# Optimization experiments

Measured on AMD Instinct MI355X. Metric: run time of the kernel, lower is better.

## Reference

```python
import jax, jax.numpy as jnp
import numpy as np

B, N, D, K = 4, 2048, 128, 32
EPS = 1e-5  # nn.LayerNorm default eps


def _lin(k, fan_in, fan_out):
    kw, kb = jax.random.split(k)
    s = 1.0 / np.sqrt(fan_in)
    w = jax.random.uniform(kw, (fan_in, fan_out), jnp.float32, -s, s)
    b = jax.random.uniform(kb, (fan_out,), jnp.float32, -s, s)
    return w, b


def setup_inputs() -> dict:
    key = jax.random.key(0)
    ks = jax.random.split(key, 3)
    inp = {}
    inp["features"] = jax.random.normal(ks[0], (B, N, D), jnp.float32)
    inp["coords"] = jax.random.uniform(ks[1], (B, N, 3), jnp.float32) * 64.0
    names = [("ql", D, D), ("kl", D, D), ("vl", D, D), ("pl1", 3, D), ("pl2", D, D),
             ("we1", D, D), ("we2", D, D), ("pe1", 3, D), ("pe2", D, D),
             ("sg1", D, D), ("sg2", D, D)]
    k2 = jax.random.split(ks[2], len(names))
    for (nm, fi, fo), kk in zip(names, k2):
        w, b = _lin(kk, fi, fo)
        inp[nm + "_w"] = w
        inp[nm + "_b"] = b
    inp["lnA_g"] = jnp.ones((D,), jnp.float32)
    inp["lnA_b"] = jnp.zeros((D,), jnp.float32)
    inp["lnF_g"] = jnp.ones((D,), jnp.float32)
    inp["lnF_b"] = jnp.zeros((D,), jnp.float32)
    return inp


def _sparsemax_k(z):
    # sparsemax over axis=1 (the K neighbor axis) of [N, K, D]
    zs = -jnp.sort(-z, axis=1)                      # descending sort
    zc = jnp.cumsum(zs, axis=1)
    r = jnp.arange(1, K + 1, dtype=z.dtype)[None, :, None]
    support = (r * zs) > (zc - 1.0)
    kz = jnp.sum(support, axis=1, keepdims=True).astype(jnp.int32)  # >= 1
    tau = (jnp.take_along_axis(zc, kz - 1, axis=1) - 1.0) / kz.astype(z.dtype)
    return jnp.maximum(z - tau, 0.0)


def _sg_prop(x, src, tgt, n):
    # SGConv (K=1) propagation: D^{-1/2}(A+I)D^{-1/2} x with self-loops added
    ar = jnp.arange(n)
    s = jnp.concatenate([src, ar])
    t = jnp.concatenate([tgt, ar])
    deg = jax.ops.segment_sum(jnp.ones(s.shape, x.dtype), t, num_segments=n)
    dinv = jax.lax.rsqrt(deg)
    norm = dinv[s] * dinv[t]
    return jax.ops.segment_sum(x[s] * norm[:, None], t, num_segments=n)


def reference(features, coords,
              ql_w, ql_b, kl_w, kl_b, vl_w, vl_b,
              pl1_w, pl1_b, pl2_w, pl2_b,
              we1_w, we1_b, we2_w, we2_b,
              lnA_g, lnA_b,
              pe1_w, pe1_b, pe2_w, pe2_b,
              sg1_w, sg1_b, sg2_w, sg2_b,
              lnF_g, lnF_b):
    def ln(x, g, b):
        m = jnp.mean(x, axis=-1, keepdims=True)
        v = jnp.var(x, axis=-1, keepdims=True)
        return (x - m) * jax.lax.rsqrt(v + EPS) * g + b

    def one(feat, coord):
        # ---- RNSA: KNN self-attention with positional embedding ----
        d2 = jnp.sum((coord[:, None, :] - coord[None, :, :]) ** 2, axis=-1)  # [N,N]
        _, idx = jax.lax.top_k(-d2, K)                   # [N,K], self included first
        diff = coord[idx] - coord[:, None, :]            # [N,K,3]
        fc = jnp.maximum(diff @ pl1_w + pl1_b, 0.0) @ pl2_w + pl2_b  # [N,K,D]
        pe = fc + feat[idx]
        Q = jnp.maximum(feat @ ql_w + ql_b, 0.0)         # [N,D]
        Kf = jnp.maximum(pe @ kl_w + kl_b, 0.0)          # [N,K,D]
        V = pe @ vl_w + vl_b
        rel = (Kf - Q[:, None, :]) * fc
        w = jnp.maximum(rel @ we1_w + we1_b, 0.0) @ we2_w + we2_b
        w = _sparsemax_k(w)                              # attn_drop is identity (eval)
        x_att = feat + jnp.einsum('nkd,nkd->nd', V, w)   # residual add
        cf = jnp.maximum(coord @ pe1_w + pe1_b, 0.0) @ pe2_w + pe2_b
        x_in = ln(x_att, lnA_g, lnA_b)
        x_pe = x_in + cf
        d2m = d2 + jnp.where(jnp.eye(N, dtype=bool), jnp.inf, 0.0)  # knn_graph: loop=False
        _, idx2 = jax.lax.top_k(-d2m, K)                 # [N,K] neighbors (sources)
        src = idx2.reshape(-1)
        tgt = jnp.repeat(jnp.arange(N), K)
        h = _sg_prop(x_pe, src, tgt, N) @ sg1_w + sg1_b
        h = jnp.maximum(h, 0.0)
        h = _sg_prop(h, src, tgt, N) @ sg2_w + sg2_b     # dropout is identity (eval)
        return ln(h + x_in, lnF_g, lnF_b)

    return jax.vmap(one)(features, coords)
```

## Files before the change

### kernel.cpp

```cpp
#include <hip/hip_runtime.h>
#include <hip/hip_bf16.h>


namespace {
constexpr int BB = 4;
constexpr int NN = 2048;
constexpr int DD = 128;
constexpr int KK = 32;
constexpr float LNEPS = 1e-5f;
constexpr int SH = 136;
constexpr int SF = 132;

constexpr int W_QL = 0, W_KL = 16384, W_VL = 32768, W_PL2 = 49152, W_WE1 = 65536,
              W_WE2 = 81920, W_PE2 = 98304, W_SG1 = 114688, W_SG2 = 131072,
              W_PL1 = 147456, W_PE1 = 147840,
              B_QL = 148224, B_KL = 148352, B_VL = 148480, B_PL1 = 148608, B_PL2 = 148736,
              B_WE1 = 148864, B_WE2 = 148992, B_PE1 = 149120, B_PE2 = 149248,
              B_SG1 = 149376, B_SG2 = 149504,
              LNA_G = 149632, LNA_B = 149760, LNF_G = 149888, LNF_B = 150016;

constexpr long OFF_FEAT  = 0;
constexpr long OFF_Q     = 1l << 20;
constexpr long OFF_XATT  = 2l << 20;
constexpr long OFF_XIN   = 3l << 20;
constexpr long OFF_XPE   = 4l << 20;
constexpr long OFF_H1    = 5l << 20;
constexpr long OFF_COORD = 6l << 20;
constexpr long OFF_W     = (6l << 20) + 32768;
constexpr long OFF_IDX   = (6l << 20) + 262144;
}

typedef __attribute__((ext_vector_type(8))) short short8;
typedef __attribute__((ext_vector_type(4))) float f32x4;

struct WPtrs { const void* p[26]; };

__device__ __forceinline__ unsigned short f2bf(float f) {
  unsigned u = __float_as_uint(f);
  return (unsigned short)((u + 0x7fffu + ((u >> 16) & 1u)) >> 16);
}
__device__ __forceinline__ float bf2f(unsigned short h) {
  return __uint_as_float(((unsigned)h) << 16);
}
__device__ __forceinline__ f32x4 mfma16(short8 a, short8 b, f32x4 c) {
  return __builtin_amdgcn_mfma_f32_16x16x32_bf16(a, b, c, 0, 0, 0);
}

__global__ void k_detect(const unsigned* __restrict__ lnAg, int* __restrict__ flag) {
  if (threadIdx.x == 0 && blockIdx.x == 0) *flag = ((lnAg[0] & 0xFFFFu) != 0u) ? 1 : 0;
}

__global__ __launch_bounds__(256) void k_convert_inputs(
    const void* __restrict__ feat, const void* __restrict__ coord, const int* __restrict__ flag,
    float* __restrict__ featf, float* __restrict__ coordf) {
  const bool isbf = (*flag != 0);
  const int nf = BB * NN * DD, nc = BB * NN * 3;
  for (int i = blockIdx.x * 256 + threadIdx.x; i < nf + nc; i += gridDim.x * 256) {
    if (i < nf) {
      featf[i] = isbf ? __bfloat162float(((const __hip_bfloat16*)feat)[i])
                      : ((const float*)feat)[i];
    } else {
      const int j = i - nf;
      coordf[j] = isbf ? __bfloat162float(((const __hip_bfloat16*)coord)[j])
                       : ((const float*)coord)[j];
    }
  }
}

__global__ __launch_bounds__(256) void k_convert_weights(WPtrs wp, const int* __restrict__ flag,
                                                         float* __restrict__ Wf) {
  const int sizes[26] = {16384,16384,16384,16384,16384,16384,16384,16384,16384,
                         384,384,
                         128,128,128,128,128,128,128,128,128,128,128,
                         128,128,128,128};
  const int offs[26] = {W_QL,W_KL,W_VL,W_PL2,W_WE1,W_WE2,W_PE2,W_SG1,W_SG2,
                        W_PL1,W_PE1,
                        B_QL,B_KL,B_VL,B_PL1,B_PL2,B_WE1,B_WE2,B_PE1,B_PE2,B_SG1,B_SG2,
                        LNA_G,LNA_B,LNF_G,LNF_B};
  const bool isbf = (*flag != 0);
  const int t = blockIdx.x;
  float* dst = Wf + offs[t];
  const int n = sizes[t];
  if (isbf) {
    const __hip_bfloat16* src = (const __hip_bfloat16*)wp.p[t];
    for (int i = threadIdx.x; i < n; i += 256) dst[i] = __bfloat162float(src[i]);
  } else {
    const float* src = (const float*)wp.p[t];
    for (int i = threadIdx.x; i < n; i += 256) dst[i] = src[i];
  }
}

__global__ __launch_bounds__(256) void k_pack(const float* __restrict__ Wf,
                                              unsigned short* __restrict__ pkH,
                                              unsigned short* __restrict__ pkL) {
  const int woffs[9] = {W_PL2, W_KL, W_VL, W_WE1, W_WE2, W_PE2, W_SG1, W_SG2, W_QL};
  const int m = blockIdx.x;
  const float* W = Wf + woffs[m];
  unsigned short* H = pkH + m * 16384;
  unsigned short* L = pkL + m * 16384;
  for (int f = threadIdx.x; f < 16384; f += 256) {
    const int j = f & 7, lane = (f >> 3) & 63, ks = (f >> 9) & 3, nt = f >> 11;
    const int k = ks * 32 + ((lane >> 4) << 3) + j, n = nt * 16 + (lane & 15);
    const float v = W[k * 128 + n];
    const unsigned short h = f2bf(v);
    H[f] = h;
    L[f] = f2bf(v - bf2f(h));
  }
}

__global__ __launch_bounds__(256) void k_knn(const float* __restrict__ coordf,
                                             int* __restrict__ idx1, int* __restrict__ idx2) {
  __shared__ float cs[NN * 3];
  __shared__ int tops[4][33];
  const int tid = threadIdx.x;
  const int wv = tid >> 6, lane = tid & 63;
  const int blk = blockIdx.x;
  const int b = blk >> 9;
  const int i = ((blk & 511) << 2) + wv;
  const float* cb = coordf + (long)b * NN * 3;
  for (int t = tid; t < NN * 3 / 4; t += 256) ((float4*)cs)[t] = ((const float4*)cb)[t];
  __syncthreads();
  const float qx = cs[i*3+0], qy = cs[i*3+1], qz = cs[i*3+2];
  float v[32];
  unsigned removed = 0u;
  float bv = 1e30f; int bj = 0x7fffffff;
  #pragma unroll
  for (int m = 0; m < 32; m++) {
    const int j = m * 64 + lane;
    const float dx = cs[j*3+0] - qx, dy = cs[j*3+1] - qy, dz = cs[j*3+2] - qz;
    const float d2 = __fadd_rn(__fadd_rn(__fmul_rn(dx,dx), __fmul_rn(dy,dy)), __fmul_rn(dz,dz));
    v[m] = d2;
    if (d2 < bv) { bv = d2; bj = j; }
  }
  for (int s = 0; s < 33; s++) {
    float mv = bv; int mj = bj;
    #pragma unroll
    for (int off = 1; off < 64; off <<= 1) {
      const float ov = __shfl_xor(mv, off, 64);
      const int   oj = __shfl_xor(mj, off, 64);
      if (ov < mv || (ov == mv && oj < mj)) { mv = ov; mj = oj; }
    }
    if (lane == 0) tops[wv][s] = mj;
    if ((mj & 63) == lane) {
      removed |= 1u << (mj >> 6);
      bv = 1e30f; bj = 0x7fffffff;
      #pragma unroll
      for (int m = 0; m < 32; m++) {
        if (!((removed >> m) & 1u) && v[m] < bv) { bv = v[m]; bj = m * 64 + lane; }
      }
    }
  }
  const unsigned long long sm = __ballot(lane < 33 && tops[wv][lane] == i);
  const int p = sm ? (__ffsll((long long)sm) - 1) : 32;
  if (lane < KK) {
    const long g = (long)b * NN + i;
    idx1[g * KK + lane] = tops[wv][lane];
    idx2[g * KK + lane] = tops[wv][lane + (lane >= p ? 1 : 0)];
  }
}

__device__ __forceinline__ void mm_core(const unsigned short* sH, const unsigned short* sL,
                                        const unsigned short* __restrict__ wH,
                                        const unsigned short* __restrict__ wL,
                                        bool useLoB, int lane, int wv, f32x4 acc[2][2]) {
  const int colq = lane & 15, quad = lane >> 4;
  #pragma unroll
  for (int mt = 0; mt < 2; ++mt) {
    const int arow = mt * 16 + colq;
    f32x4 a0 = {0.f, 0.f, 0.f, 0.f}, a1 = {0.f, 0.f, 0.f, 0.f};
    #pragma unroll
    for (int ks = 0; ks < 4; ++ks) {
      const short8 ah = *(const short8*)(sH + arow * SH + ks * 32 + quad * 8);
      const short8 al = *(const short8*)(sL + arow * SH + ks * 32 + quad * 8);
      const int nt0 = 2 * wv, nt1 = 2 * wv + 1;
      const short8 b0 = *(const short8*)(wH + ((nt0 * 4 + ks) * 64 + lane) * 8);
      const short8 b1 = *(const short8*)(wH + ((nt1 * 4 + ks) * 64 + lane) * 8);
      a0 = mfma16(ah, b0, a0);
      a0 = mfma16(al, b0, a0);
      a1 = mfma16(ah, b1, a1);
      a1 = mfma16(al, b1, a1);
      if (useLoB) {
        const short8 bl0 = *(const short8*)(wL + ((nt0 * 4 + ks) * 64 + lane) * 8);
        const short8 bl1 = *(const short8*)(wL + ((nt1 * 4 + ks) * 64 + lane) * 8);
        a0 = mfma16(ah, bl0, a0);
        a1 = mfma16(ah, bl1, a1);
      }
    }
    acc[mt][0] = a0;
    acc[mt][1] = a1;
  }
}

__device__ __forceinline__ void split_store2(unsigned short* H, unsigned short* L,
                                             int row0, int col, float v0, float v1) {
  float2 vv; vv.x = v0; vv.y = v1;
  const __hip_bfloat162 h2 = __float22bfloat162_rn(vv);
  float2 ll; ll.x = v0 - __bfloat162float(h2.x); ll.y = v1 - __bfloat162float(h2.y);
  const __hip_bfloat162 l2 = __float22bfloat162_rn(ll);
  *(__hip_bfloat16*)(H + row0 * SH + col) = h2.x;
  *(__hip_bfloat16*)(H + (row0 + 1) * SH + col) = h2.y;
  *(__hip_bfloat16*)(L + row0 * SH + col) = l2.x;
  *(__hip_bfloat16*)(L + (row0 + 1) * SH + col) = l2.y;
}

__device__ __forceinline__ void split_store_row16(unsigned short* H, unsigned short* L,
                                                  int row, int c0, const float* v) {
  #pragma unroll
  for (int h2 = 0; h2 < 2; ++h2) {
    short8 oh, ol;
    #pragma unroll
    for (int e = 0; e < 8; ++e) {
      const float x = v[h2 * 8 + e];
      const unsigned short h = f2bf(x);
      oh[e] = (short)h; ol[e] = (short)f2bf(x - bf2f(h));
    }
    *(short8*)(H + row * SH + c0 + h2 * 8) = oh;
    *(short8*)(L + row * SH + c0 + h2 * 8) = ol;
  }
}

__global__ __launch_bounds__(256) void k_q(const float* __restrict__ featf,
                                           const float* __restrict__ Wf,
                                           const unsigned short* __restrict__ pkH,
                                           const unsigned short* __restrict__ pkL,
                                           const int* __restrict__ flag,
                                           float* __restrict__ Qm) {
  __shared__ __align__(16) unsigned short AH[KK*SH], AL[KK*SH];
  const int tid = threadIdx.x;
  const int lane = tid & 63, wv = tid >> 6;
  const int colq = lane & 15, quad = lane >> 4;
  const bool useLoB = (*flag == 0);
  const int row8 = tid >> 3, c0 = (tid & 7) * 16;
  const long gg0 = (long)blockIdx.x * 32;
  float s[16];
  {
    const float* sp = featf + (gg0 + row8) * DD + c0;
    #pragma unroll
    for (int e = 0; e < 16; e += 4) {
      const float4 v = *(const float4*)(sp + e);
      s[e] = v.x; s[e+1] = v.y; s[e+2] = v.z; s[e+3] = v.w;
    }
  }
  split_store_row16(AH, AL, row8, c0, s);
  __syncthreads();
  f32x4 acc[2][2];
  mm_core(AH, AL, pkH + 8*16384, pkL + 8*16384, useLoB, lane, wv, acc);
  #pragma unroll
  for (int ntl = 0; ntl < 2; ++ntl) {
    const int col = (2*wv + ntl)*16 + colq;
    const float bv = Wf[B_QL + col];
    #pragma unroll
    for (int mt = 0; mt < 2; ++mt) {
      const int rowb = mt*16 + quad*4;
      #pragma unroll
      for (int r = 0; r < 4; ++r)
        Qm[(gg0 + rowb + r) * DD + col] = fmaxf(acc[mt][ntl][r] + bv, 0.f);
    }
  }
}

__global__ __launch_bounds__(256, 2) void k_attn(const float* __restrict__ featf,
                                              const float* __restrict__ coordf,
                                              const float* __restrict__ Qm,
                                              const int* __restrict__ idx1,
                                              const float* __restrict__ Wf,
                                              const unsigned short* __restrict__ pkH,
                                              const unsigned short* __restrict__ pkL,
                                              const int* __restrict__ flag,
                                              float* __restrict__ x_att) {
  __shared__ __align__(16) unsigned short AH[KK*SH], AL[KK*SH], CH[KK*SH], CL[KK*SH];
  __shared__ int nb[KK];
  __shared__ float Fs[DD];
  const int tid = threadIdx.x;
  const int lane = tid & 63, wv = tid >> 6;
  const int colq = lane & 15, quad = lane >> 4;
  const int g = blockIdx.x; const int i = g & (NN - 1); const int b = g >> 11;
  const long bN = (long)b * NN;
  const bool useLoB = (*flag == 0);
  if (tid < KK) nb[tid] = idx1[(long)g * KK + tid];
  if (tid < DD) Fs[tid] = featf[(bN + i) * DD + tid];
  __syncthreads();
  const int row8 = tid >> 3, c0 = (tid & 7) * 16;

  {
    const float* cb = coordf + (long)b * NN * 3;
    const int j = nb[row8];
    const float dx = cb[j*3+0] - cb[i*3+0], dy = cb[j*3+1] - cb[i*3+1], dz = cb[j*3+2] - cb[i*3+2];
    float t1v[16];
    #pragma unroll
    for (int c4 = 0; c4 < 4; ++c4) {
      const int cc = c0 + c4*4;
      const float4 w0 = *(const float4*)(Wf + W_PL1 + cc);
      const float4 w1 = *(const float4*)(Wf + W_PL1 + 128 + cc);
      const float4 w2 = *(const float4*)(Wf + W_PL1 + 256 + cc);
      const float4 bp = *(const float4*)(Wf + B_PL1 + cc);
      t1v[c4*4+0] = fmaxf(fmaf(dz,w2.x,fmaf(dy,w1.x,fmaf(dx,w0.x,bp.x))), 0.f);
      t1v[c4*4+1] = fmaxf(fmaf(dz,w2.y,fmaf(dy,w1.y,fmaf(dx,w0.y,bp.y))), 0.f);
      t1v[c4*4+2] = fmaxf(fmaf(dz,w2.z,fmaf(dy,w1.z,fmaf(dx,w0.z,bp.z))), 0.f);
      t1v[c4*4+3] = fmaxf(fmaf(dz,w2.w,fmaf(dy,w1.w,fmaf(dx,w0.w,bp.w))), 0.f);
    }
    split_store_row16(AH, AL, row8, c0, t1v);
  }
  __syncthreads();
  f32x4 acc[2][2];
  float fc[2][2][4];
  {
    mm_core(AH, AL, pkH + 0*16384, pkL + 0*16384, useLoB, lane, wv, acc);
    #pragma unroll
    for (int ntl = 0; ntl < 2; ++ntl) {
      const int col = (2*wv + ntl)*16 + colq;
      const float bv = Wf[B_PL2 + col];
      #pragma unroll
      for (int mt = 0; mt < 2; ++mt) {
        const int rowb = mt*16 + quad*4;
        float pe[4];
        #pragma unroll
        for (int r = 0; r < 4; ++r) {
          const float f = acc[mt][ntl][r] + bv;
          fc[mt][ntl][r] = f;
          pe[r] = f + featf[(bN + nb[rowb + r]) * DD + col];
        }
        split_store2(CH, CL, rowb + 0, col, pe[0], pe[1]);
        split_store2(CH, CL, rowb + 2, col, pe[2], pe[3]);
      }
    }
  }
  __syncthreads();
  {
    mm_core(CH, CL, pkH + 1*16384, pkL + 1*16384, useLoB, lane, wv, acc);
    #pragma unroll
    for (int ntl = 0; ntl < 2; ++ntl) {
      const int col = (2*wv + ntl)*16 + colq;
      const float bv = Wf[B_KL + col];
      const float qv = Qm[(bN + i) * DD + col];
      #pragma unroll
      for (int mt = 0; mt < 2; ++mt) {
        const int rowb = mt*16 + quad*4;
        float rel[4];
        #pragma unroll
        for (int r = 0; r < 4; ++r) {
          const float kf = fmaxf(acc[mt][ntl][r] + bv, 0.f);
          rel[r] = (kf - qv) * fc[mt][ntl][r];
        }
        split_store2(AH, AL, rowb + 0, col, rel[0], rel[1]);
        split_store2(AH, AL, rowb + 2, col, rel[2], rel[3]);
      }
    }
  }
  f32x4 Vacc[2][2];
  mm_core(CH, CL, pkH + 2*16384, pkL + 2*16384, useLoB, lane, wv, Vacc);
  __syncthreads();
  {
    mm_core(AH, AL, pkH + 3*16384, pkL + 3*16384, useLoB, lane, wv, acc);
    #pragma unroll
    for (int ntl = 0; ntl < 2; ++ntl) {
      const int col = (2*wv + ntl)*16 + colq;
      const float bv = Wf[B_WE1 + col];
      #pragma unroll
      for (int mt = 0; mt < 2; ++mt) {
        const int rowb = mt*16 + quad*4;
        split_store2(CH, CL, rowb + 0, col,
                     fmaxf(acc[mt][ntl][0] + bv, 0.f), fmaxf(acc[mt][ntl][1] + bv, 0.f));
        split_store2(CH, CL, rowb + 2, col,
                     fmaxf(acc[mt][ntl][2] + bv, 0.f), fmaxf(acc[mt][ntl][3] + bv, 0.f));
      }
    }
  }
  __syncthreads();
  f32x4 Wacc[2][2];
  mm_core(CH, CL, pkH + 4*16384, pkL + 4*16384, useLoB, lane, wv, Wacc);

  #pragma unroll
  for (int ntl = 0; ntl < 2; ++ntl) {
    const int col = (2*wv + ntl)*16 + colq;
    const float bw = Wf[B_WE2 + col];
    const float bvv = Wf[B_VL + col];
    float z[8], Vv[8];
    #pragma unroll
    for (int mt = 0; mt < 2; ++mt)
      #pragma unroll
      for (int r = 0; r < 4; ++r) {
        z[mt*4+r]  = Wacc[mt][ntl][r] + bw;
        Vv[mt*4+r] = Vacc[mt][ntl][r] + bvv;
      }
    float S = 0.f;
    #pragma unroll
    for (int e = 0; e < 8; ++e) S += z[e];
    S += __shfl_xor(S, 16, 64); S += __shfl_xor(S, 32, 64);
    float tau = (S - 1.0f) * (1.0f / 32.0f);
    int cnt = 32;
    for (int it = 0; it < 40; ++it) {
      float s = 0.f; int c = 0;
      #pragma unroll
      for (int e = 0; e < 8; ++e) { if (z[e] > tau) { s += z[e]; c++; } }
      s += __shfl_xor(s, 16, 64); s += __shfl_xor(s, 32, 64);
      c += __shfl_xor(c, 16, 64); c += __shfl_xor(c, 32, 64);
      const float ntau = (s - 1.0f) / (float)c;
      const int changed = (c != cnt);
      cnt = c; tau = ntau;
      if (!__any(changed)) break;
    }
    float pv = 0.f;
    #pragma unroll
    for (int e = 0; e < 8; ++e) pv = fmaf(fmaxf(z[e] - tau, 0.f), Vv[e], pv);
    pv += __shfl_xor(pv, 16, 64); pv += __shfl_xor(pv, 32, 64);
    if (quad == 0) x_att[(bN + i) * DD + col] = Fs[col] + pv;
  }
}

__global__ __launch_bounds__(256) void k_lnA_pe(const float* __restrict__ x_att,
                                                const float* __restrict__ coordf,
                                                const float* __restrict__ Wf,
                                                const unsigned short* __restrict__ pkH,
                                                const unsigned short* __restrict__ pkL,
                                                const int* __restrict__ flag,
                                                float* __restrict__ x_in, float* __restrict__ x_pe) {
  __shared__ __align__(16) unsigned short AH[KK*SH], AL[KK*SH];
  __shared__ float Xf[KK][SF];
  const int tid = threadIdx.x;
  const int lane = tid & 63, wv = tid >> 6;
  const int colq = lane & 15, quad = lane >> 4;
  const bool useLoB = (*flag == 0);
  const int row8 = tid >> 3, c0 = (tid & 7) * 16;
  const long gg0 = (long)blockIdx.x * 32;
  const long gr = gg0 + row8;
  const int b = (int)(gr >> 11), i = (int)(gr & (NN - 1));

  float xa[16];
  {
    const float* xr = x_att + gr * DD + c0;
    #pragma unroll
    for (int e = 0; e < 16; e += 4) {
      const float4 v = *(const float4*)(xr + e);
      xa[e] = v.x; xa[e+1] = v.y; xa[e+2] = v.z; xa[e+3] = v.w;
    }
  }
  float sm = 0.f, s2 = 0.f;
  #pragma unroll
  for (int e = 0; e < 16; ++e) { sm += xa[e]; s2 = fmaf(xa[e], xa[e], s2); }
  #pragma unroll
  for (int off = 1; off < 8; off <<= 1) {
    sm += __shfl_xor(sm, off, 64);
    s2 += __shfl_xor(s2, off, 64);
  }
  const float m = sm * (1.f/128.f);
  const float var = s2 * (1.f/128.f) - m * m;
  const float rstd = rsqrtf(var + LNEPS);
  float xin[16];
  #pragma unroll
  for (int e = 0; e < 16; ++e) {
    xin[e] = (xa[e] - m) * rstd * Wf[LNA_G + c0 + e] + Wf[LNA_B + c0 + e];
    Xf[row8][c0 + e] = xin[e];
  }
  #pragma unroll
  for (int e = 0; e < 16; e += 4) {
    float4 v; v.x = xin[e]; v.y = xin[e+1]; v.z = xin[e+2]; v.w = xin[e+3];
    *(float4*)(x_in + gr * DD + c0 + e) = v;
  }
  {
    const float* cp = coordf + ((long)b * NN + i) * 3;
    const float cx = cp[0], cy = cp[1], cz = cp[2];
    float tv[16];
    #pragma unroll
    for (int c4 = 0; c4 < 4; ++c4) {
      const int cc = c0 + c4*4;
      const float4 w0 = *(const float4*)(Wf + W_PE1 + cc);
      const float4 w1 = *(const float4*)(Wf + W_PE1 + 128 + cc);
      const float4 w2 = *(const float4*)(Wf + W_PE1 + 256 + cc);
      const float4 bp = *(const float4*)(Wf + B_PE1 + cc);
      tv[c4*4+0] = fmaxf(fmaf(cz,w2.x,fmaf(cy,w1.x,fmaf(cx,w0.x,bp.x))), 0.f);
      tv[c4*4+1] = fmaxf(fmaf(cz,w2.y,fmaf(cy,w1.y,fmaf(cx,w0.y,bp.y))), 0.f);
      tv[c4*4+2] = fmaxf(fmaf(cz,w2.z,fmaf(cy,w1.z,fmaf(cx,w0.z,bp.z))), 0.f);
      tv[c4*4+3] = fmaxf(fmaf(cz,w2.w,fmaf(cy,w1.w,fmaf(cx,w0.w,bp.w))), 0.f);
    }
    split_store_row16(AH, AL, row8, c0, tv);
  }
  __syncthreads();
  f32x4 acc[2][2];
  mm_core(AH, AL, pkH + 5*16384, pkL + 5*16384, useLoB, lane, wv, acc);
  #pragma unroll
  for (int ntl = 0; ntl < 2; ++ntl) {
    const int col = (2*wv + ntl)*16 + colq;
    const float bv = Wf[B_PE2 + col];
    #pragma unroll
    for (int mt = 0; mt < 2; ++mt) {
      const int rowb = mt*16 + quad*4;
      #pragma unroll
      for (int r = 0; r < 4; ++r)
        x_pe[(gg0 + rowb + r) * DD + col] = Xf[rowb + r][col] + acc[mt][ntl][r] + bv;
    }
  }
}

__global__ __launch_bounds__(256) void k_sg1(const float* __restrict__ x_pe,
                                             const int* __restrict__ idx2,
                                             const float* __restrict__ Wf,
                                             const unsigned short* __restrict__ pkH,
                                             const unsigned short* __restrict__ pkL,
                                             const int* __restrict__ flag,
                                             float* __restrict__ h1) {
  __shared__ __align__(16) unsigned short AH[KK*SH], AL[KK*SH];
  __shared__ int nb2[32][KK];
  const int tid = threadIdx.x;
  const int lane = tid & 63, wv = tid >> 6;
  const int colq = lane & 15, quad = lane >> 4;
  const bool useLoB = (*flag == 0);
  const int row8 = tid >> 3, c0 = (tid & 7) * 16;
  const long gg0 = (long)blockIdx.x * 32;
  const long bN = (gg0 >> 11) << 11;
  for (int t = tid; t < 32 * KK; t += 256)
    nb2[t >> 5][t & 31] = idx2[(gg0 + (t >> 5)) * KK + (t & 31)];
  __syncthreads();
  float s[16];
  {
    const float* sp = x_pe + (gg0 + row8) * DD + c0;
    #pragma unroll
    for (int e = 0; e < 16; e += 4) {
      const float4 v = *(const float4*)(sp + e);
      s[e] = v.x; s[e+1] = v.y; s[e+2] = v.z; s[e+3] = v.w;
    }
  }
  for (int k = 0; k < KK; ++k) {
    const float* np_ = x_pe + (bN + nb2[row8][k]) * DD + c0;
    #pragma unroll
    for (int e = 0; e < 16; e += 4) {
      const float4 v = *(const float4*)(np_ + e);
      s[e] += v.x; s[e+1] += v.y; s[e+2] += v.z; s[e+3] += v.w;
    }
  }
  #pragma unroll
  for (int e = 0; e < 16; ++e) s[e] *= (1.f / 33.f);
  split_store_row16(AH, AL, row8, c0, s);
  __syncthreads();
  f32x4 acc[2][2];
  mm_core(AH, AL, pkH + 6*16384, pkL + 6*16384, useLoB, lane, wv, acc);
  #pragma unroll
  for (int ntl = 0; ntl < 2; ++ntl) {
    const int col = (2*wv + ntl)*16 + colq;
    const float bv = Wf[B_SG1 + col];
    #pragma unroll
    for (int mt = 0; mt < 2; ++mt) {
      const int rowb = mt*16 + quad*4;
      #pragma unroll
      for (int r = 0; r < 4; ++r)
        h1[(gg0 + rowb + r) * DD + col] = fmaxf(acc[mt][ntl][r] + bv, 0.f);
    }
  }
}

__global__ __launch_bounds__(256) void k_sg2(const float* __restrict__ h1,
                                             const int* __restrict__ idx2,
                                             const float* __restrict__ x_in,
                                             const float* __restrict__ Wf,
                                             const unsigned short* __restrict__ pkH,
                                             const unsigned short* __restrict__ pkL,
                                             const int* __restrict__ flag,
                                             void* __restrict__ out) {
  __shared__ __align__(16) unsigned short AH[KK*SH], AL[KK*SH];
  __shared__ float Yf[KK][SF];
  __shared__ int nb2[32][KK];
  const int tid = threadIdx.x;
  const int lane = tid & 63, wv = tid >> 6;
  const int colq = lane & 15, quad = lane >> 4;
  const bool isbf = (*flag != 0);
  const bool useLoB = !isbf;
  const int row8 = tid >> 3, c0 = (tid & 7) * 16;
  const long gg0 = (long)blockIdx.x * 32;
  const long bN = (gg0 >> 11) << 11;
  for (int t = tid; t < 32 * KK; t += 256)
    nb2[t >> 5][t & 31] = idx2[(gg0 + (t >> 5)) * KK + (t & 31)];
  __syncthreads();
  float s[16];
  {
    const float* sp = h1 + (gg0 + row8) * DD + c0;
    #pragma unroll
    for (int e = 0; e < 16; e += 4) {
      const float4 v = *(const float4*)(sp + e);
      s[e] = v.x; s[e+1] = v.y; s[e+2] = v.z; s[e+3] = v.w;
    }
  }
  for (int k = 0; k < KK; ++k) {
    const float* np_ = h1 + (bN + nb2[row8][k]) * DD + c0;
    #pragma unroll
    for (int e = 0; e < 16; e += 4) {
      const float4 v = *(const float4*)(np_ + e);
      s[e] += v.x; s[e+1] += v.y; s[e+2] += v.z; s[e+3] += v.w;
    }
  }
  #pragma unroll
  for (int e = 0; e < 16; ++e) s[e] *= (1.f / 33.f);
  split_store_row16(AH, AL, row8, c0, s);
  __syncthreads();
  f32x4 acc[2][2];
  mm_core(AH, AL, pkH + 7*16384, pkL + 7*16384, useLoB, lane, wv, acc);
  #pragma unroll
  for (int ntl = 0; ntl < 2; ++ntl) {
    const int col = (2*wv + ntl)*16 + colq;
    const float bv = Wf[B_SG2 + col];
    #pragma unroll
    for (int mt = 0; mt < 2; ++mt) {
      const int rowb = mt*16 + quad*4;
      #pragma unroll
      for (int r = 0; r < 4; ++r)
        Yf[rowb + r][col] = acc[mt][ntl][r] + bv + x_in[(gg0 + rowb + r) * DD + col];
    }
  }
  __syncthreads();
  float y[16];
  #pragma unroll
  for (int e = 0; e < 16; ++e) y[e] = Yf[row8][c0 + e];
  float sm = 0.f, s2 = 0.f;
  #pragma unroll
  for (int e = 0; e < 16; ++e) { sm += y[e]; s2 = fmaf(y[e], y[e], s2); }
  #pragma unroll
  for (int off = 1; off < 8; off <<= 1) {
    sm += __shfl_xor(sm, off, 64);
    s2 += __shfl_xor(s2, off, 64);
  }
  const float m = sm * (1.f/128.f);
  const float var = s2 * (1.f/128.f) - m * m;
  const float rstd = rsqrtf(var + LNEPS);
  const long gr = gg0 + row8;
  #pragma unroll
  for (int e = 0; e < 16; ++e) {
    const float o = (y[e] - m) * rstd * Wf[LNF_G + c0 + e] + Wf[LNF_B + c0 + e];
    if (isbf) ((__hip_bfloat16*)out)[gr * DD + c0 + e] = __float2bfloat16(o);
    else      ((float*)out)[gr * DD + c0 + e] = o;
  }
}

extern "C" void kernel_launch(void* const* d_in, const int* in_sizes, int n_in,
                              void* d_out, int out_size, void* d_ws, size_t ws_size,
                              hipStream_t stream) {
  float* ws = (float*)d_ws;
  float* featf  = ws + OFF_FEAT;
  float* Qm     = ws + OFF_Q;
  float* x_att  = ws + OFF_XATT;
  float* x_in   = ws + OFF_XIN;
  float* x_pe   = ws + OFF_XPE;
  float* h1     = ws + OFF_H1;
  float* coordf = ws + OFF_COORD;
  float* Wf     = ws + OFF_W;
  int* idx1 = (int*)(ws + OFF_IDX);
  int* idx2 = idx1 + (long)BB * NN * KK;
  int* flag = idx2 + (long)BB * NN * KK;
  unsigned short* pkH = (unsigned short*)(flag + 64);
  unsigned short* pkL = pkH + 9 * 16384;

  WPtrs wp;
  const int map[26] = {2,4,6,10,12,14,18,20,22, 8,16,
                       3,5,7,9,11,13,15,17,19,21,23,
                       24,25,26,27};
  for (int t = 0; t < 26; t++) wp.p[t] = d_in[map[t]];

  k_detect<<<1, 64, 0, stream>>>((const unsigned*)d_in[24], flag);
  k_convert_inputs<<<2048, 256, 0, stream>>>(d_in[0], d_in[1], flag, featf, coordf);
  k_convert_weights<<<26, 256, 0, stream>>>(wp, flag, Wf);
  k_pack<<<9, 256, 0, stream>>>(Wf, pkH, pkL);
  k_knn<<<BB * NN / 4, 256, 0, stream>>>(coordf, idx1, idx2);
  k_q<<<BB * NN / 32, 256, 0, stream>>>(featf, Wf, pkH, pkL, flag, Qm);
  k_attn<<<BB * NN, 256, 0, stream>>>(featf, coordf, Qm, idx1, Wf, pkH, pkL, flag, x_att);
  k_lnA_pe<<<BB * NN / 32, 256, 0, stream>>>(x_att, coordf, Wf, pkH, pkL, flag, x_in, x_pe);
  k_sg1<<<BB * NN / 32, 256, 0, stream>>>(x_pe, idx2, Wf, pkH, pkL, flag, h1);
  k_sg2<<<BB * NN / 32, 256, 0, stream>>>(h1, idx2, x_in, Wf, pkH, pkL, flag, (void*)d_out);
}
```

Before: 486.8 us.

## Switch split-bf16 matmuls to fp16 activations, fuse knn with Q, drop detect kernel

```diff
diff --git a/kernel.cpp b/kernel.cpp
--- a/kernel.cpp
+++ b/kernel.cpp
@@ -30,30 +30,23 @@
 constexpr long OFF_IDX   = (6l << 20) + 262144;
 }
 
-typedef __attribute__((ext_vector_type(8))) short short8;
+typedef _Float16 f16;
+typedef __attribute__((ext_vector_type(8))) _Float16 half8;
 typedef __attribute__((ext_vector_type(4))) float f32x4;
 
 struct WPtrs { const void* p[26]; };
 
-__device__ __forceinline__ unsigned short f2bf(float f) {
-  unsigned u = __float_as_uint(f);
-  return (unsigned short)((u + 0x7fffu + ((u >> 16) & 1u)) >> 16);
-}
-__device__ __forceinline__ float bf2f(unsigned short h) {
-  return __uint_as_float(((unsigned)h) << 16);
-}
-__device__ __forceinline__ f32x4 mfma16(short8 a, short8 b, f32x4 c) {
-  return __builtin_amdgcn_mfma_f32_16x16x32_bf16(a, b, c, 0, 0, 0);
-}
-
-__global__ void k_detect(const unsigned* __restrict__ lnAg, int* __restrict__ flag) {
-  if (threadIdx.x == 0 && blockIdx.x == 0) *flag = ((lnAg[0] & 0xFFFFu) != 0u) ? 1 : 0;
+__device__ __forceinline__ f32x4 mfma16h(half8 a, half8 b, f32x4 c) {
+  return __builtin_amdgcn_mfma_f32_16x16x32_f16(a, b, c, 0, 0, 0);
+}
+__device__ __forceinline__ bool bf_inputs(const unsigned* __restrict__ dt) {
+  return (dt[0] & 0xFFFFu) != 0u;
 }
 
 __global__ __launch_bounds__(256) void k_convert_inputs(
-    const void* __restrict__ feat, const void* __restrict__ coord, const int* __restrict__ flag,
+    const void* __restrict__ feat, const void* __restrict__ coord, const unsigned* __restrict__ dt,
     float* __restrict__ featf, float* __restrict__ coordf) {
-  const bool isbf = (*flag != 0);
+  const bool isbf = bf_inputs(dt);
   const int nf = BB * NN * DD, nc = BB * NN * 3;
   for (int i = blockIdx.x * 256 + threadIdx.x; i < nf + nc; i += gridDim.x * 256) {
     if (i < nf) {
@@ -67,7 +60,7 @@
   }
 }
 
-__global__ __launch_bounds__(256) void k_convert_weights(WPtrs wp, const int* __restrict__ flag,
+__global__ __launch_bounds__(256) void k_convert_weights(WPtrs wp, const unsigned* __restrict__ dt,
                                                          float* __restrict__ Wf) {
   const int sizes[26] = {16384,16384,16384,16384,16384,16384,16384,16384,16384,
                          384,384,
@@ -77,7 +70,7 @@
                         W_PL1,W_PE1,
                         B_QL,B_KL,B_VL,B_PL1,B_PL2,B_WE1,B_WE2,B_PE1,B_PE2,B_SG1,B_SG2,
                         LNA_G,LNA_B,LNF_G,LNF_B};
-  const bool isbf = (*flag != 0);
+  const bool isbf = bf_inputs(dt);
   const int t = blockIdx.x;
   float* dst = Wf + offs[t];
   const int n = sizes[t];
@@ -91,78 +84,26 @@
 }
 
 __global__ __launch_bounds__(256) void k_pack(const float* __restrict__ Wf,
-                                              unsigned short* __restrict__ pkH,
-                                              unsigned short* __restrict__ pkL) {
+                                              f16* __restrict__ pkH, f16* __restrict__ pkL) {
   const int woffs[9] = {W_PL2, W_KL, W_VL, W_WE1, W_WE2, W_PE2, W_SG1, W_SG2, W_QL};
   const int m = blockIdx.x;
   const float* W = Wf + woffs[m];
-  unsigned short* H = pkH + m * 16384;
-  unsigned short* L = pkL + m * 16384;
+  f16* H = pkH + m * 16384;
+  f16* L = pkL + m * 16384;
   for (int f = threadIdx.x; f < 16384; f += 256) {
     const int j = f & 7, lane = (f >> 3) & 63, ks = (f >> 9) & 3, nt = f >> 11;
     const int k = ks * 32 + ((lane >> 4) << 3) + j, n = nt * 16 + (lane & 15);
     const float v = W[k * 128 + n];
-    const unsigned short h = f2bf(v);
+    const f16 h = (f16)v;
     H[f] = h;
-    L[f] = f2bf(v - bf2f(h));
-  }
-}
-
-__global__ __launch_bounds__(256) void k_knn(const float* __restrict__ coordf,
-                                             int* __restrict__ idx1, int* __restrict__ idx2) {
-  __shared__ float cs[NN * 3];
-  __shared__ int tops[4][33];
-  const int tid = threadIdx.x;
-  const int wv = tid >> 6, lane = tid & 63;
-  const int blk = blockIdx.x;
-  const int b = blk >> 9;
-  const int i = ((blk & 511) << 2) + wv;
-  const float* cb = coordf + (long)b * NN * 3;
-  for (int t = tid; t < NN * 3 / 4; t += 256) ((float4*)cs)[t] = ((const float4*)cb)[t];
-  __syncthreads();
-  const float qx = cs[i*3+0], qy = cs[i*3+1], qz = cs[i*3+2];
-  float v[32];
-  unsigned removed = 0u;
-  float bv = 1e30f; int bj = 0x7fffffff;
-  #pragma unroll
-  for (int m = 0; m < 32; m++) {
-    const int j = m * 64 + lane;
-    const float dx = cs[j*3+0] - qx, dy = cs[j*3+1] - qy, dz = cs[j*3+2] - qz;
-    const float d2 = __fadd_rn(__fadd_rn(__fmul_rn(dx,dx), __fmul_rn(dy,dy)), __fmul_rn(dz,dz));
-    v[m] = d2;
-    if (d2 < bv) { bv = d2; bj = j; }
-  }
-  for (int s = 0; s < 33; s++) {
-    float mv = bv; int mj = bj;
-    #pragma unroll
-    for (int off = 1; off < 64; off <<= 1) {
-      const float ov = __shfl_xor(mv, off, 64);
-      const int   oj = __shfl_xor(mj, off, 64);
-      if (ov < mv || (ov == mv && oj < mj)) { mv = ov; mj = oj; }
-    }
-    if (lane == 0) tops[wv][s] = mj;
-    if ((mj & 63) == lane) {
-      removed |= 1u << (mj >> 6);
-      bv = 1e30f; bj = 0x7fffffff;
-      #pragma unroll
-      for (int m = 0; m < 32; m++) {
-        if (!((removed >> m) & 1u) && v[m] < bv) { bv = v[m]; bj = m * 64 + lane; }
-      }
-    }
-  }
-  const unsigned long long sm = __ballot(lane < 33 && tops[wv][lane] == i);
-  const int p = sm ? (__ffsll((long long)sm) - 1) : 32;
-  if (lane < KK) {
-    const long g = (long)b * NN + i;
-    idx1[g * KK + lane] = tops[wv][lane];
-    idx2[g * KK + lane] = tops[wv][lane + (lane >= p ? 1 : 0)];
-  }
-}
-
-__device__ __forceinline__ void mm_core(const unsigned short* sH, const unsigned short* sL,
-                                        const unsigned short* __restrict__ wH,
-                                        const unsigned short* __restrict__ wL,
-                                        bool useLoB, int lane, int wv, f32x4 acc[2][2]) {
+    L[f] = (f16)(v - (float)h);
+  }
+}
+
+__device__ __forceinline__ void mm_core(const f16* sA,
+                                        const f16* __restrict__ wH,
+                                        const f16* __restrict__ wL,
+                                        bool useLoW, int lane, int wv, f32x4 acc[2][2]) {
   const int colq = lane & 15, quad = lane >> 4;
   #pragma unroll
   for (int mt = 0; mt < 2; ++mt) {
@@ -170,20 +111,17 @@
     f32x4 a0 = {0.f, 0.f, 0.f, 0.f}, a1 = {0.f, 0.f, 0.f, 0.f};
     #pragma unroll
     for (int ks = 0; ks < 4; ++ks) {
-      const short8 ah = *(const short8*)(sH + arow * SH + ks * 32 + quad * 8);
-      const short8 al = *(const short8*)(sL + arow * SH + ks * 32 + quad * 8);
+      const half8 a = *(const half8*)(sA + arow * SH + ks * 32 + quad * 8);
       const int nt0 = 2 * wv, nt1 = 2 * wv + 1;
-      const short8 b0 = *(const short8*)(wH + ((nt0 * 4 + ks) * 64 + lane) * 8);
-      const short8 b1 = *(const short8*)(wH + ((nt1 * 4 + ks) * 64 + lane) * 8);
-      a0 = mfma16(ah, b0, a0);
-      a0 = mfma16(al, b0, a0);
-      a1 = mfma16(ah, b1, a1);
-      a1 = mfma16(al, b1, a1);
-      if (useLoB) {
-        const short8 bl0 = *(const short8*)(wL + ((nt0 * 4 + ks) * 64 + lane) * 8);
-        const short8 bl1 = *(const short8*)(wL + ((nt1 * 4 + ks) * 64 + lane) * 8);
-        a0 = mfma16(ah, bl0, a0);
-        a1 = mfma16(ah, bl1, a1);
+      const half8 b0 = *(const half8*)(wH + ((nt0 * 4 + ks) * 64 + lane) * 8);
+      const half8 b1 = *(const half8*)(wH + ((nt1 * 4 + ks) * 64 + lane) * 8);
+      a0 = mfma16h(a, b0, a0);
+      a1 = mfma16h(a, b1, a1);
+      if (useLoW) {
+        const half8 bl0 = *(const half8*)(wL + ((nt0 * 4 + ks) * 64 + lane) * 8);
+        const half8 bl1 = *(const half8*)(wL + ((nt1 * 4 + ks) * 64 + lane) * 8);
+        a0 = mfma16h(a, bl0, a0);
+        a1 = mfma16h(a, bl1, a1);
       }
     }
     acc[mt][0] = a0;
@@ -191,84 +129,119 @@
   }
 }
 
-__device__ __forceinline__ void split_store2(unsigned short* H, unsigned short* L,
-                                             int row0, int col, float v0, float v1) {
-  float2 vv; vv.x = v0; vv.y = v1;
-  const __hip_bfloat162 h2 = __float22bfloat162_rn(vv);
-  float2 ll; ll.x = v0 - __bfloat162float(h2.x); ll.y = v1 - __bfloat162float(h2.y);
-  const __hip_bfloat162 l2 = __float22bfloat162_rn(ll);
-  *(__hip_bfloat16*)(H + row0 * SH + col) = h2.x;
-  *(__hip_bfloat16*)(H + (row0 + 1) * SH + col) = h2.y;
-  *(__hip_bfloat16*)(L + row0 * SH + col) = l2.x;
-  *(__hip_bfloat16*)(L + (row0 + 1) * SH + col) = l2.y;
-}
-
-__device__ __forceinline__ void split_store_row16(unsigned short* H, unsigned short* L,
-                                                  int row, int c0, const float* v) {
-  #pragma unroll
-  for (int h2 = 0; h2 < 2; ++h2) {
-    short8 oh, ol;
-    #pragma unroll
-    for (int e = 0; e < 8; ++e) {
-      const float x = v[h2 * 8 + e];
-      const unsigned short h = f2bf(x);
-      oh[e] = (short)h; ol[e] = (short)f2bf(x - bf2f(h));
-    }
-    *(short8*)(H + row * SH + c0 + h2 * 8) = oh;
-    *(short8*)(L + row * SH + c0 + h2 * 8) = ol;
-  }
-}
-
-__global__ __launch_bounds__(256) void k_q(const float* __restrict__ featf,
-                                           const float* __restrict__ Wf,
-                                           const unsigned short* __restrict__ pkH,
-                                           const unsigned short* __restrict__ pkL,
-                                           const int* __restrict__ flag,
-                                           float* __restrict__ Qm) {
-  __shared__ __align__(16) unsigned short AH[KK*SH], AL[KK*SH];
+__device__ __forceinline__ void h_store2(f16* A, int row0, int col, float v0, float v1) {
+  A[row0 * SH + col] = (f16)v0;
+  A[(row0 + 1) * SH + col] = (f16)v1;
+}
+
+__device__ __forceinline__ void h_store_row16(f16* A, int row, int c0, const float* v) {
+  half8 o0, o1;
+  #pragma unroll
+  for (int e = 0; e < 8; ++e) { o0[e] = (f16)v[e]; o1[e] = (f16)v[8 + e]; }
+  *(half8*)(A + row * SH + c0) = o0;
+  *(half8*)(A + row * SH + c0 + 8) = o1;
+}
+
+__global__ __launch_bounds__(256) void k_knn_q(const float* __restrict__ coordf,
+                                               const float* __restrict__ featf,
+                                               const float* __restrict__ Wf,
+                                               const f16* __restrict__ pkH,
+                                               const f16* __restrict__ pkL,
+                                               const unsigned* __restrict__ dt,
+                                               int* __restrict__ idx1, int* __restrict__ idx2,
+                                               float* __restrict__ Qm) {
+  __shared__ __align__(16) unsigned char smem[NN * 3 * 4 + 4 * 33 * 4];
   const int tid = threadIdx.x;
-  const int lane = tid & 63, wv = tid >> 6;
-  const int colq = lane & 15, quad = lane >> 4;
-  const bool useLoB = (*flag == 0);
-  const int row8 = tid >> 3, c0 = (tid & 7) * 16;
-  const long gg0 = (long)blockIdx.x * 32;
-  float s[16];
-  {
+  if (blockIdx.x < 2048) {
+    float* cs = (float*)smem;
+    int (*tops)[33] = (int(*)[33])(smem + NN * 3 * 4);
+    const int wv = tid >> 6, lane = tid & 63;
+    const int blk = blockIdx.x;
+    const int b = blk >> 9;
+    const int i = ((blk & 511) << 2) + wv;
+    const float* cb = coordf + (long)b * NN * 3;
+    for (int t = tid; t < NN * 3 / 4; t += 256) ((float4*)cs)[t] = ((const float4*)cb)[t];
+    __syncthreads();
+    const float qx = cs[i*3+0], qy = cs[i*3+1], qz = cs[i*3+2];
+    float v[32];
+    unsigned removed = 0u;
+    float bv = 1e30f; int bj = 0x7fffffff;
+    #pragma unroll
+    for (int m = 0; m < 32; m++) {
+      const int j = m * 64 + lane;
+      const float dx = cs[j*3+0] - qx, dy = cs[j*3+1] - qy, dz = cs[j*3+2] - qz;
+      const float d2 = __fadd_rn(__fadd_rn(__fmul_rn(dx,dx), __fmul_rn(dy,dy)), __fmul_rn(dz,dz));
+      v[m] = d2;
+      if (d2 < bv) { bv = d2; bj = j; }
+    }
+    for (int s = 0; s < 33; s++) {
+      float mv = bv; int mj = bj;
+      #pragma unroll
+      for (int off = 1; off < 64; off <<= 1) {
+        const float ov = __shfl_xor(mv, off, 64);
+        const int   oj = __shfl_xor(mj, off, 64);
+        if (ov < mv || (ov == mv && oj < mj)) { mv = ov; mj = oj; }
+      }
+      if (lane == 0) tops[wv][s] = mj;
+      if ((mj & 63) == lane) {
+        removed |= 1u << (mj >> 6);
+        bv = 1e30f; bj = 0x7fffffff;
+        #pragma unroll
+        for (int m = 0; m < 32; m++) {
+          if (!((removed >> m) & 1u) && v[m] < bv) { bv = v[m]; bj = m * 64 + lane; }
+        }
+      }
+    }
+    const unsigned long long sm = __ballot(lane < 33 && tops[wv][lane] == i);
+    const int p = sm ? (__ffsll((long long)sm) - 1) : 32;
+    if (lane < KK) {
+      const long g = (long)b * NN + i;
+      idx1[g * KK + lane] = tops[wv][lane];
+      idx2[g * KK + lane] = tops[wv][lane + (lane >= p ? 1 : 0)];
+    }
+  } else {
+    f16* AH = (f16*)smem;
+    const int lane = tid & 63, wv = tid >> 6;
+    const int colq = lane & 15, quad = lane >> 4;
+    const bool useLoW = !bf_inputs(dt);
+    const int row8 = tid >> 3, c0 = (tid & 7) * 16;
+    const long gg0 = (long)(blockIdx.x - 2048) * 32;
+    float s[16];
     const float* sp = featf + (gg0 + row8) * DD + c0;
     #pragma unroll
     for (int e = 0; e < 16; e += 4) {
-      const float4 v = *(const float4*)(sp + e);
-      s[e] = v.x; s[e+1] = v.y; s[e+2] = v.z; s[e+3] = v.w;
-    }
-  }
-  split_store_row16(AH, AL, row8, c0, s);
-  __syncthreads();
-  f32x4 acc[2][2];
-  mm_core(AH, AL, pkH + 8*16384, pkL + 8*16384, useLoB, lane, wv, acc);
-  #pragma unroll
-  for (int ntl = 0; ntl < 2; ++ntl) {
-    const int col = (2*wv + ntl)*16 + colq;
-    const float bv = Wf[B_QL + col];
-    #pragma unroll
-    for (int mt = 0; mt < 2; ++mt) {
-      const int rowb = mt*16 + quad*4;
-      #pragma unroll
-      for (int r = 0; r < 4; ++r)
-        Qm[(gg0 + rowb + r) * DD + col] = fmaxf(acc[mt][ntl][r] + bv, 0.f);
-    }
-  }
-}
-
-__global__ __launch_bounds__(256, 2) void k_attn(const float* __restrict__ featf,
+      const float4 vv = *(const float4*)(sp + e);
+      s[e] = vv.x; s[e+1] = vv.y; s[e+2] = vv.z; s[e+3] = vv.w;
+    }
+    h_store_row16(AH, row8, c0, s);
+    __syncthreads();
+    f32x4 acc[2][2];
+    mm_core(AH, pkH + 8*16384, pkL + 8*16384, useLoW, lane, wv, acc);
+    #pragma unroll
+    for (int ntl = 0; ntl < 2; ++ntl) {
+      const int col = (2*wv + ntl)*16 + colq;
+      const float bv = Wf[B_QL + col];
+      #pragma unroll
+      for (int mt = 0; mt < 2; ++mt) {
+        const int rowb = mt*16 + quad*4;
+        #pragma unroll
+        for (int r = 0; r < 4; ++r)
+          Qm[(gg0 + rowb + r) * DD + col] = fmaxf(acc[mt][ntl][r] + bv, 0.f);
+      }
+    }
+  }
+}
+
+__global__ __launch_bounds__(256, 4) void k_attn(const float* __restrict__ featf,
                                               const float* __restrict__ coordf,
                                               const float* __restrict__ Qm,
                                               const int* __restrict__ idx1,
                                               const float* __restrict__ Wf,
-                                              const unsigned short* __restrict__ pkH,
-                                              const unsigned short* __restrict__ pkL,
-                                              const int* __restrict__ flag,
+                                              const f16* __restrict__ pkH,
+                                              const f16* __restrict__ pkL,
+                                              const unsigned* __restrict__ dt,
                                               float* __restrict__ x_att) {
-  __shared__ __align__(16) unsigned short AH[KK*SH], AL[KK*SH], CH[KK*SH], CL[KK*SH];
+  __shared__ __align__(16) f16 AH[KK*SH], CH[KK*SH];
   __shared__ int nb[KK];
   __shared__ float Fs[DD];
   const int tid = threadIdx.x;
@@ -276,7 +249,7 @@
   const int colq = lane & 15, quad = lane >> 4;
   const int g = blockIdx.x; const int i = g & (NN - 1); const int b = g >> 11;
   const long bN = (long)b * NN;
-  const bool useLoB = (*flag == 0);
+  const bool useLoW = !bf_inputs(dt);
   if (tid < KK) nb[tid] = idx1[(long)g * KK + tid];
   if (tid < DD) Fs[tid] = featf[(bN + i) * DD + tid];
   __syncthreads();
@@ -299,13 +272,13 @@
       t1v[c4*4+2] = fmaxf(fmaf(dz,w2.z,fmaf(dy,w1.z,fmaf(dx,w0.z,bp.z))), 0.f);
       t1v[c4*4+3] = fmaxf(fmaf(dz,w2.w,fmaf(dy,w1.w,fmaf(dx,w0.w,bp.w))), 0.f);
     }
-    split_store_row16(AH, AL, row8, c0, t1v);
+    h_store_row16(AH, row8, c0, t1v);
   }
   __syncthreads();
   f32x4 acc[2][2];
   float fc[2][2][4];
   {
-    mm_core(AH, AL, pkH + 0*16384, pkL + 0*16384, useLoB, lane, wv, acc);
+    mm_core(AH, pkH + 0*16384, pkL + 0*16384, useLoW, lane, wv, acc);
     #pragma unroll
     for (int ntl = 0; ntl < 2; ++ntl) {
       const int col = (2*wv + ntl)*16 + colq;
@@ -320,14 +293,14 @@
           fc[mt][ntl][r] = f;
           pe[r] = f + featf[(bN + nb[rowb + r]) * DD + col];
         }
-        split_store2(CH, CL, rowb + 0, col, pe[0], pe[1]);
-        split_store2(CH, CL, rowb + 2, col, pe[2], pe[3]);
-      }
-    }
-  }
-  __syncthreads();
-  {
-    mm_core(CH, CL, pkH + 1*16384, pkL + 1*16384, useLoB, lane, wv, acc);
+        h_store2(CH, rowb + 0, col, pe[0], pe[1]);
+        h_store2(CH, rowb + 2, col, pe[2], pe[3]);
+      }
+    }
+  }
+  __syncthreads();
+  {
+    mm_core(CH, pkH + 1*16384, pkL + 1*16384, useLoW, lane, wv, acc);
     #pragma unroll
     for (int ntl = 0; ntl < 2; ++ntl) {
       const int col = (2*wv + ntl)*16 + colq;
@@ -342,16 +315,16 @@
           const float kf = fmaxf(acc[mt][ntl][r] + bv, 0.f);
           rel[r] = (kf - qv) * fc[mt][ntl][r];
         }
-        split_store2(AH, AL, rowb + 0, col, rel[0], rel[1]);
-        split_store2(AH, AL, rowb + 2, col, rel[2], rel[3]);
+        h_store2(AH, rowb + 0, col, rel[0], rel[1]);
+        h_store2(AH, rowb + 2, col, rel[2], rel[3]);
       }
     }
   }
   f32x4 Vacc[2][2];
-  mm_core(CH, CL, pkH + 2*16384, pkL + 2*16384, useLoB, lane, wv, Vacc);
-  __syncthreads();
-  {
-    mm_core(AH, AL, pkH + 3*16384, pkL + 3*16384, useLoB, lane, wv, acc);
+  mm_core(CH, pkH + 2*16384, pkL + 2*16384, useLoW, lane, wv, Vacc);
+  __syncthreads();
+  {
+    mm_core(AH, pkH + 3*16384, pkL + 3*16384, useLoW, lane, wv, acc);
     #pragma unroll
     for (int ntl = 0; ntl < 2; ++ntl) {
       const int col = (2*wv + ntl)*16 + colq;
@@ -359,16 +332,16 @@
       #pragma unroll
       for (int mt = 0; mt < 2; ++mt) {
         const int rowb = mt*16 + quad*4;
-        split_store2(CH, CL, rowb + 0, col,
-                     fmaxf(acc[mt][ntl][0] + bv, 0.f), fmaxf(acc[mt][ntl][1] + bv, 0.f));
-        split_store2(CH, CL, rowb + 2, col,
-                     fmaxf(acc[mt][ntl][2] + bv, 0.f), fmaxf(acc[mt][ntl][3] + bv, 0.f));
+        h_store2(CH, rowb + 0, col,
+                 fmaxf(acc[mt][ntl][0] + bv, 0.f), fmaxf(acc[mt][ntl][1] + bv, 0.f));
+        h_store2(CH, rowb + 2, col,
+                 fmaxf(acc[mt][ntl][2] + bv, 0.f), fmaxf(acc[mt][ntl][3] + bv, 0.f));
       }
     }
   }
   __syncthreads();
   f32x4 Wacc[2][2];
-  mm_core(CH, CL, pkH + 4*16384, pkL + 4*16384, useLoB, lane, wv, Wacc);
+  mm_core(CH, pkH + 4*16384, pkL + 4*16384, useLoW, lane, wv, Wacc);
 
   #pragma unroll
   for (int ntl = 0; ntl < 2; ++ntl) {
@@ -411,16 +384,16 @@
 __global__ __launch_bounds__(256) void k_lnA_pe(const float* __restrict__ x_att,
                                                 const float* __restrict__ coordf,
                                                 const float* __restrict__ Wf,
-                                                const unsigned short* __restrict__ pkH,
-                                                const unsigned short* __restrict__ pkL,
-                                                const int* __restrict__ flag,
+                                                const f16* __restrict__ pkH,
+                                                const f16* __restrict__ pkL,
+                                                const unsigned* __restrict__ dt,
                                                 float* __restrict__ x_in, float* __restrict__ x_pe) {
-  __shared__ __align__(16) unsigned short AH[KK*SH], AL[KK*SH];
+  __shared__ __align__(16) f16 AH[KK*SH];
   __shared__ float Xf[KK][SF];
   const int tid = threadIdx.x;
   const int lane = tid & 63, wv = tid >> 6;
   const int colq = lane & 15, quad = lane >> 4;
-  const bool useLoB = (*flag == 0);
+  const bool useLoW = !bf_inputs(dt);
   const int row8 = tid >> 3, c0 = (tid & 7) * 16;
   const long gg0 = (long)blockIdx.x * 32;
   const long gr = gg0 + row8;
@@ -473,11 +446,11 @@
       tv[c4*4+2] = fmaxf(fmaf(cz,w2.z,fmaf(cy,w1.z,fmaf(cx,w0.z,bp.z))), 0.f);
       tv[c4*4+3] = fmaxf(fmaf(cz,w2.w,fmaf(cy,w1.w,fmaf(cx,w0.w,bp.w))), 0.f);
     }
-    split_store_row16(AH, AL, row8, c0, tv);
+    h_store_row16(AH, row8, c0, tv);
   }
   __syncthreads();
   f32x4 acc[2][2];
-  mm_core(AH, AL, pkH + 5*16384, pkL + 5*16384, useLoB, lane, wv, acc);
+  mm_core(AH, pkH + 5*16384, pkL + 5*16384, useLoW, lane, wv, acc);
   #pragma unroll
   for (int ntl = 0; ntl < 2; ++ntl) {
     const int col = (2*wv + ntl)*16 + colq;
@@ -495,16 +468,16 @@
 __global__ __launch_bounds__(256) void k_sg1(const float* __restrict__ x_pe,
                                              const int* __restrict__ idx2,
                                              const float* __restrict__ Wf,
-                                             const unsigned short* __restrict__ pkH,
-                                             const unsigned short* __restrict__ pkL,
-                                             const int* __restrict__ flag,
+                                             const f16* __restrict__ pkH,
+                                             const f16* __restrict__ pkL,
+                                             const unsigned* __restrict__ dt,
                                              float* __restrict__ h1) {
-  __shared__ __align__(16) unsigned short AH[KK*SH], AL[KK*SH];
+  __shared__ __align__(16) f16 AH[KK*SH];
   __shared__ int nb2[32][KK];
   const int tid = threadIdx.x;
   const int lane = tid & 63, wv = tid >> 6;
   const int colq = lane & 15, quad = lane >> 4;
-  const bool useLoB = (*flag == 0);
+  const bool useLoW = !bf_inputs(dt);
   const int row8 = tid >> 3, c0 = (tid & 7) * 16;
   const long gg0 = (long)blockIdx.x * 32;
   const long bN = (gg0 >> 11) << 11;
@@ -530,10 +503,10 @@
   }
   #pragma unroll
   for (int e = 0; e < 16; ++e) s[e] *= (1.f / 33.f);
-  split_store_row16(AH, AL, row8, c0, s);
+  h_store_row16(AH, row8, c0, s);
   __syncthreads();
   f32x4 acc[2][2];
-  mm_core(AH, AL, pkH + 6*16384, pkL + 6*16384, useLoB, lane, wv, acc);
+  mm_core(AH, pkH + 6*16384, pkL + 6*16384, useLoW, lane, wv, acc);
   #pragma unroll
   for (int ntl = 0; ntl < 2; ++ntl) {
     const int col = (2*wv + ntl)*16 + colq;
@@ -552,18 +525,18 @@
                                              const int* __restrict__ idx2,
                                              const float* __restrict__ x_in,
                                              const float* __restrict__ Wf,
-                                             const unsigned short* __restrict__ pkH,
-                                             const unsigned short* __restrict__ pkL,
-                                             const int* __restrict__ flag,
+                                             const f16* __restrict__ pkH,
+                                             const f16* __restrict__ pkL,
+                                             const unsigned* __restrict__ dt,
                                              void* __restrict__ out) {
-  __shared__ __align__(16) unsigned short AH[KK*SH], AL[KK*SH];
+  __shared__ __align__(16) f16 AH[KK*SH];
   __shared__ float Yf[KK][SF];
   __shared__ int nb2[32][KK];
   const int tid = threadIdx.x;
   const int lane = tid & 63, wv = tid >> 6;
   const int colq = lane & 15, quad = lane >> 4;
-  const bool isbf = (*flag != 0);
-  const bool useLoB = !isbf;
+  const bool isbf = bf_inputs(dt);
+  const bool useLoW = !isbf;
   const int row8 = tid >> 3, c0 = (tid & 7) * 16;
   const long gg0 = (long)blockIdx.x * 32;
   const long bN = (gg0 >> 11) << 11;
@@ -589,10 +562,10 @@
   }
   #pragma unroll
   for (int e = 0; e < 16; ++e) s[e] *= (1.f / 33.f);
-  split_store_row16(AH, AL, row8, c0, s);
+  h_store_row16(AH, row8, c0, s);
   __syncthreads();
   f32x4 acc[2][2];
-  mm_core(AH, AL, pkH + 7*16384, pkL + 7*16384, useLoB, lane, wv, acc);
+  mm_core(AH, pkH + 7*16384, pkL + 7*16384, useLoW, lane, wv, acc);
   #pragma unroll
   for (int ntl = 0; ntl < 2; ++ntl) {
     const int col = (2*wv + ntl)*16 + colq;
@@ -643,9 +616,9 @@
   float* Wf     = ws + OFF_W;
   int* idx1 = (int*)(ws + OFF_IDX);
   int* idx2 = idx1 + (long)BB * NN * KK;
-  int* flag = idx2 + (long)BB * NN * KK;
-  unsigned short* pkH = (unsigned short*)(flag + 64);
-  unsigned short* pkL = pkH + 9 * 16384;
+  f16* pkH = (f16*)(idx2 + (long)BB * NN * KK);
+  f16* pkL = pkH + 9 * 16384;
+  const unsigned* dt = (const unsigned*)d_in[24];
 
   WPtrs wp;
   const int map[26] = {2,4,6,10,12,14,18,20,22, 8,16,
@@ -653,14 +626,13 @@
                        24,25,26,27};
   for (int t = 0; t < 26; t++) wp.p[t] = d_in[map[t]];
 
-  k_detect<<<1, 64, 0, stream>>>((const unsigned*)d_in[24], flag);
-  k_convert_inputs<<<2048, 256, 0, stream>>>(d_in[0], d_in[1], flag, featf, coordf);
-  k_convert_weights<<<26, 256, 0, stream>>>(wp, flag, Wf);
+  k_convert_inputs<<<2048, 256, 0, stream>>>(d_in[0], d_in[1], dt, featf, coordf);
+  k_convert_weights<<<26, 256, 0, stream>>>(wp, dt, Wf);
   k_pack<<<9, 256, 0, stream>>>(Wf, pkH, pkL);
-  k_knn<<<BB * NN / 4, 256, 0, stream>>>(coordf, idx1, idx2);
-  k_q<<<BB * NN / 32, 256, 0, stream>>>(featf, Wf, pkH, pkL, flag, Qm);
-  k_attn<<<BB * NN, 256, 0, stream>>>(featf, coordf, Qm, idx1, Wf, pkH, pkL, flag, x_att);
-  k_lnA_pe<<<BB * NN / 32, 256, 0, stream>>>(x_att, coordf, Wf, pkH, pkL, flag, x_in, x_pe);
-  k_sg1<<<BB * NN / 32, 256, 0, stream>>>(x_pe, idx2, Wf, pkH, pkL, flag, h1);
-  k_sg2<<<BB * NN / 32, 256, 0, stream>>>(h1, idx2, x_in, Wf, pkH, pkL, flag, (void*)d_out);
-}
+  k_knn_q<<<BB * NN / 4 + BB * NN / 32, 256, 0, stream>>>(coordf, featf, Wf, pkH, pkL, dt,
+                                                          idx1, idx2, Qm);
+  k_attn<<<BB * NN, 256, 0, stream>>>(featf, coordf, Qm, idx1, Wf, pkH, pkL, dt, x_att);
+  k_lnA_pe<<<BB * NN / 32, 256, 0, stream>>>(x_att, coordf, Wf, pkH, pkL, dt, x_in, x_pe);
+  k_sg1<<<BB * NN / 32, 256, 0, stream>>>(x_pe, idx2, Wf, pkH, pkL, dt, h1);
+  k_sg2<<<BB * NN / 32, 256, 0, stream>>>(h1, idx2, x_in, Wf, pkH, pkL, dt, (void*)d_out);
+}
```

After: 485.4 us. About the same (-0.3%).
